# Performance work log

Measured on AMD Instinct MI355X. Metric: run time of the kernel, lower is better.

## Reference

```python
import jax, jax.numpy as jnp
import numpy as np

B, T, D = 2, 2048, 1024
H, HS = 16, 64
EPS = 1e-5

def _ln(x, g, b):
    m = jnp.mean(x, axis=-1, keepdims=True)
    v = jnp.mean((x - m) ** 2, axis=-1, keepdims=True)
    return (x - m) * jax.lax.rsqrt(v + EPS) * g + b

def setup_inputs() -> dict:
    key = jax.random.key(0)
    ks = jax.random.split(key, 8)
    s_in = 1.0 / np.sqrt(D)
    s_ff = 1.0 / np.sqrt(4 * D)
    return {
        "embds": jax.random.normal(ks[0], (B, T, D), jnp.float32),
        "Wq": jax.random.normal(ks[1], (H, D, HS), jnp.float32) * s_in,
        "Wk": jax.random.normal(ks[2], (H, D, HS), jnp.float32) * s_in,
        "Wv": jax.random.normal(ks[3], (H, D, HS), jnp.float32) * s_in,
        "ln1_g": jnp.ones((D,), jnp.float32),
        "ln1_b": jnp.zeros((D,), jnp.float32),
        "ln2_g": jnp.ones((D,), jnp.float32),
        "ln2_b": jnp.zeros((D,), jnp.float32),
        "W1": jax.random.normal(ks[4], (D, 4 * D), jnp.float32) * s_in,
        "b1": jnp.zeros((4 * D,), jnp.float32),
        "W2": jax.random.normal(ks[5], (4 * D, D), jnp.float32) * s_ff,
        "b2": jnp.zeros((D,), jnp.float32),
    }

def reference(embds, Wq, Wk, Wv, ln1_g, ln1_b, ln2_g, ln2_b, W1, b1, W2, b2):
    _, t, d = embds.shape
    x = _ln(embds, ln1_g, ln1_b)
    q = jnp.einsum("btd,hde->bhte", x, Wq)
    k = jnp.einsum("btd,hde->bhte", x, Wk)
    v = jnp.einsum("btd,hde->bhte", x, Wv)
    # NOTE: repo scales by num_embds**-0.5 (C of input), not head_size**-0.5
    scores = jnp.einsum("bhte,bhse->bhts", q, k) * (d ** -0.5)
    causal = jnp.tril(jnp.ones((t, t), bool))
    scores = jnp.where(causal, scores, -jnp.inf)
    w = jax.nn.softmax(scores, axis=-1)
    o = jnp.einsum("bhts,bhse->bhte", w, v)  # [B,H,T,HS]
    attn = o.transpose(0, 2, 1, 3).reshape(embds.shape[0], t, -1)  # concat heads
    embds = embds + attn
    y = _ln(embds, ln2_g, ln2_b)
    ff = jax.nn.relu(y @ W1 + b1) @ W2 + b2
    return embds + ff
```

## Files before the change

### kernel.cpp

```cpp
#include <hip/hip_runtime.h>

using s16x8 = __attribute__((ext_vector_type(8))) short;
using f32x4 = __attribute__((ext_vector_type(4))) float;
typedef unsigned int   u32;
typedef unsigned short u16;

__device__ __forceinline__ u16 f2bf(float f) {
  u32 u = __float_as_uint(f);
  u += 0x7fffu + ((u >> 16) & 1u);
  return (u16)(u >> 16);
}
__device__ __forceinline__ float bf2f(u16 s) {
  return __uint_as_float(((u32)s) << 16);
}

typedef __attribute__((address_space(1))) const unsigned int g_u32;
typedef __attribute__((address_space(3))) unsigned int l_u32;
__device__ __forceinline__ void gload16(const void* g, void* l) {
  __builtin_amdgcn_global_load_lds((g_u32*)g, (l_u32*)l, 16, 0, 0);
}

#define WAITB(N) asm volatile("s_waitcnt vmcnt(" #N ")\ns_barrier" ::: "memory")
#define BAR()    asm volatile("s_barrier" ::: "memory")

__device__ __forceinline__ size_t kfrag_addr(int bh, int t, int e) {
  const int pair = (((t >> 4) & 3) << 1) + (e >> 5);
  const int slot = ((e >> 3) & 3) * 16 + (t & 15);
  return ((((size_t)bh * 32 + (t >> 6)) * 8 + pair) * 64 + slot) * 8 + (e & 7);
}
__device__ __forceinline__ size_t vfrag_addr(int bh, int t, int e) {
  const int pair = (((e >> 4) & 3) << 1) + ((t >> 5) & 1);
  const int slot = ((t >> 3) & 3) * 16 + (e & 15);
  return ((((size_t)bh * 32 + (t >> 6)) * 8 + pair) * 64 + slot) * 8 + (t & 7);
}

__global__ __launch_bounds__(256) void transpose_pack(
    const float* __restrict__ src, u16* __restrict__ dst, int R, int C)
{
  __shared__ u16 tile[64][66];
  const int tid = threadIdx.x;
  const int c0 = blockIdx.x * 64, r0 = blockIdx.y * 64;
  const size_t zoff = (size_t)blockIdx.z * R * C;
  src += zoff; dst += zoff;
  const int rr = tid >> 6, cc = tid & 63;
  #pragma unroll
  for (int i = 0; i < 16; ++i)
    tile[i * 4 + rr][cc] = f2bf(src[(size_t)(r0 + i * 4 + rr) * C + c0 + cc]);
  __syncthreads();
  #pragma unroll
  for (int i = 0; i < 16; ++i)
    dst[(size_t)(c0 + i * 4 + rr) * R + r0 + cc] = tile[cc][i * 4 + rr];
}

__global__ __launch_bounds__(256) void transpose_qkv(
    const float* __restrict__ Wq, const float* __restrict__ Wk,
    const float* __restrict__ Wv, u16* __restrict__ dst)
{
  __shared__ u16 tile[64][66];
  const int tid = threadIdx.x;
  const int sel = blockIdx.z >> 4, head = blockIdx.z & 15;
  const int r0 = blockIdx.y * 64;
  const float* src = ((sel == 0) ? Wq : (sel == 1) ? Wk : Wv) + (size_t)head * 65536;
  u16* d = dst + ((size_t)sel << 20) + (size_t)head * 65536;
  const int rr = tid >> 6, cc = tid & 63;
  #pragma unroll
  for (int i = 0; i < 16; ++i)
    tile[i * 4 + rr][cc] = f2bf(src[(size_t)(r0 + i * 4 + rr) * 64 + cc]);
  __syncthreads();
  #pragma unroll
  for (int i = 0; i < 16; ++i)
    d[(size_t)(i * 4 + rr) * 1024 + r0 + cc] = tile[cc][i * 4 + rr];
}

__global__ __launch_bounds__(256) void ln_kernel(
    const float* __restrict__ x, const float* __restrict__ g,
    const float* __restrict__ be, u16* __restrict__ out)
{
  const int row = blockIdx.x, tid = threadIdx.x;
  const int lane = tid & 63, wave = tid >> 6;
  const float4 v = ((const float4*)(x + (size_t)row * 1024))[tid];
  float s  = v.x + v.y + v.z + v.w;
  float sq = v.x * v.x + v.y * v.y + v.z * v.z + v.w * v.w;
  #pragma unroll
  for (int m = 1; m < 64; m <<= 1) { s += __shfl_xor(s, m); sq += __shfl_xor(sq, m); }
  __shared__ float rs[4], rq[4];
  if (lane == 0) { rs[wave] = s; rq[wave] = sq; }
  __syncthreads();
  s  = rs[0] + rs[1] + rs[2] + rs[3];
  sq = rq[0] + rq[1] + rq[2] + rq[3];
  const float mean = s * (1.0f / 1024.0f);
  const float var  = sq * (1.0f / 1024.0f) - mean * mean;
  const float rstd = rsqrtf(var + 1e-5f);
  const int c = tid * 4;
  const float4 gv = ((const float4*)g)[tid];
  const float4 bv = ((const float4*)be)[tid];
  ushort4 o;
  o.x = f2bf((v.x - mean) * rstd * gv.x + bv.x);
  o.y = f2bf((v.y - mean) * rstd * gv.y + bv.y);
  o.z = f2bf((v.z - mean) * rstd * gv.z + bv.z);
  o.w = f2bf((v.w - mean) * rstd * gv.w + bv.w);
  *(ushort4*)&out[(size_t)row * 1024 + c] = o;
}

#define MFMA_Q(MQ, NH)                                                        \
  do {                                                                        \
    __builtin_amdgcn_s_setprio(1);                                            \
    _Pragma("unroll") for (int m_ = 0; m_ < 4; ++m_)                          \
      _Pragma("unroll") for (int n_ = 0; n_ < 2; ++n_)                        \
        _Pragma("unroll") for (int ks_ = 0; ks_ < 2; ++ks_)                   \
          acc[MQ * 4 + m_][NH * 2 + n_] =                                     \
            __builtin_amdgcn_mfma_f32_16x16x32_bf16(                          \
              aF[m_][ks_], (NH ? b1F : b0F)[n_][ks_],                         \
              acc[MQ * 4 + m_][NH * 2 + n_], 0, 0, 0);                        \
    __builtin_amdgcn_s_setprio(0);                                            \
  } while (0)

template<int MODE>
__global__ __launch_bounds__(512, 2) void gemm256(
    const u16* __restrict__ A, int lda, const u16* __restrict__ BT, int ldb,
    int K, u16* __restrict__ o1, const float* __restrict__ bias,
    u16* __restrict__ pout, u16* __restrict__ o0q, u16* __restrict__ o0k,
    u16* __restrict__ o0v)
{
  __shared__ alignas(16) u16 lds[2][2][256 * 64];
  const int tid = threadIdx.x, lane = tid & 63, w = tid >> 6;
  const int wm = w >> 2, wn = w & 3;
  const int fr = lane & 15, g = lane >> 4;
  const int gx = gridDim.x, nwg = gx * gridDim.y;
  int lid = blockIdx.y * gx + blockIdx.x;
  lid = (lid & 7) * (nwg >> 3) + (lid >> 3);
  const int col0 = (lid % gx) * 256, row0 = (lid / gx) * 256;
  const int koff = (MODE == 3) ? blockIdx.z * 1024 : 0;
  if constexpr (MODE == 3) pout += (size_t)blockIdx.z * (4096 * 1024);

  const int srow = w * 16 + (lane >> 3);
  const int scol8 = (lane & 7) ^ ((lane >> 3) & 7);
  const u16* Ab = A  + (size_t)(row0 + srow) * lda + koff + scol8 * 8;
  const u16* Bb = BT + (size_t)(col0 + srow) * ldb + koff + scol8 * 8;
  const int sdst = (w * 16) * 64 + lane * 8;

  const int x7 = fr & 7;
  const int rA = wm * 128 + fr;
  const int rB = wn * 64 + fr;

  f32x4 acc[8][4] = {};
  s16x8 aF[4][2], b0F[2][2], b1F[2][2];
  const int nkt = K >> 6;

  auto stA = [&](int buf, int half, int kt) {
    #pragma unroll
    for (int g2 = 0; g2 < 2; ++g2)
      gload16(Ab + (size_t)(half * 128 + g2 * 8) * lda + kt * 64,
              &lds[buf][0][(half * 128 + g2 * 8) * 64 + sdst]);
  };
  auto stB = [&](int buf, int half, int kt) {
    #pragma unroll
    for (int g2 = 0; g2 < 2; ++g2)
      gload16(Bb + (size_t)(half * 128 + g2 * 8) * ldb + kt * 64,
              &lds[buf][1][(half * 128 + g2 * 8) * 64 + sdst]);
  };
  auto rdA = [&](int buf, int mq) {
    #pragma unroll
    for (int m = 0; m < 4; ++m)
      #pragma unroll
      for (int ks = 0; ks < 2; ++ks)
        aF[m][ks] = *(const s16x8*)
          &lds[buf][0][(rA + mq * 64 + m * 16) * 64 + ((ks * 4 + g) ^ x7) * 8];
  };
  auto rdB0 = [&](int buf) {
    #pragma unroll
    for (int n = 0; n < 2; ++n)
      #pragma unroll
      for (int ks = 0; ks < 2; ++ks)
        b0F[n][ks] = *(const s16x8*)
          &lds[buf][1][(rB + n * 16) * 64 + ((ks * 4 + g) ^ x7) * 8];
  };
  auto rdB1 = [&](int buf) {
    #pragma unroll
    for (int n = 0; n < 2; ++n)
      #pragma unroll
      for (int ks = 0; ks < 2; ++ks)
        b1F[n][ks] = *(const s16x8*)
          &lds[buf][1][(rB + (n + 2) * 16) * 64 + ((ks * 4 + g) ^ x7) * 8];
  };

  stA(0, 0, 0); stA(0, 1, 0); stB(0, 0, 0); stB(0, 1, 0);
  stA(1, 0, 1); stA(1, 1, 1); stB(1, 0, 1); stB(1, 1, 1);
  WAITB(8);

  const int niter = nkt >> 1;
  for (int i = 0; i < niter; ++i) {
    #pragma unroll
    for (int half = 0; half < 2; ++half) {
      const int buf = half;
      const int skt = 2 * i + 2 + half;
      const bool st = (skt < nkt);
      rdA(buf, 0); rdB0(buf);
      BAR();
      MFMA_Q(0, 0);
      BAR();
      rdB1(buf);
      if (st) stB(buf, 0, skt);
      BAR();
      MFMA_Q(0, 1);
      BAR();
      rdA(buf, 1);
      if (st) stA(buf, 0, skt);
      BAR();
      MFMA_Q(1, 0);
      BAR();
      if (st) { stA(buf, 1, skt); stB(buf, 1, skt); }
      BAR();
      MFMA_Q(1, 1);
      WAITB(6);
    }
  }

  const float QSCALE = 0.03125f * 1.4426950408889634f;
  #pragma unroll
  for (int m8 = 0; m8 < 8; ++m8) {
    const int rbase = row0 + wm * 128 + m8 * 16 + g * 4;
    #pragma unroll
    for (int n4 = 0; n4 < 4; ++n4) {
      const int col = col0 + wn * 64 + n4 * 16 + fr;
      if constexpr (MODE == 0) {
        const int ww = col >> 10, h = (col >> 6) & 15, e = col & 63;
        const int b = rbase >> 11, t0 = rbase & 2047;
        const int bh = b * 16 + h;
        if (ww == 0) {
          #pragma unroll
          for (int j = 0; j < 4; ++j)
            o0q[((size_t)bh * 2048 + (t0 + j)) * 64 + e] =
              f2bf(acc[m8][n4][j] * QSCALE);
        } else if (ww == 1) {
          #pragma unroll
          for (int j = 0; j < 4; ++j)
            o0k[kfrag_addr(bh, t0 + j, e)] = f2bf(acc[m8][n4][j]);
        } else {
          ushort4 pk;
          pk.x = f2bf(acc[m8][n4][0]); pk.y = f2bf(acc[m8][n4][1]);
          pk.z = f2bf(acc[m8][n4][2]); pk.w = f2bf(acc[m8][n4][3]);
          *(ushort4*)&o0v[vfrag_addr(bh, t0, e)] = pk;
        }
      } else if constexpr (MODE == 1) {
        const float bb = bias[col];
        #pragma unroll
        for (int j = 0; j < 4; ++j)
          o1[(size_t)(rbase + j) * 4096 + col] =
            f2bf(fmaxf(acc[m8][n4][j] + bb, 0.0f));
      } else {
        #pragma unroll
        for (int j = 0; j < 4; ++j)
          pout[(size_t)(rbase + j) * 1024 + col] = f2bf(acc[m8][n4][j]);
      }
    }
  }
}

__global__ __launch_bounds__(256) void ff2_reduce(
    const u16* __restrict__ pbuf, const float* __restrict__ e2,
    const float* __restrict__ b2, float* __restrict__ out)
{
  const int i4 = blockIdx.x * 256 + threadIdx.x;
  const int row = i4 >> 8, c4 = i4 & 255;
  float4 a = ((const float4*)e2)[i4];
  const float4 bb = ((const float4*)b2)[c4];
  a.x += bb.x; a.y += bb.y; a.z += bb.z; a.w += bb.w;
  #pragma unroll
  for (int z = 0; z < 4; ++z) {
    const ushort4 p = *(const ushort4*)
      &pbuf[(size_t)z * (4096 * 1024) + (size_t)row * 1024 + c4 * 4];
    a.x += bf2f(p.x); a.y += bf2f(p.y); a.z += bf2f(p.z); a.w += bf2f(p.w);
  }
  ((float4*)out)[i4] = a;
}

__global__ __launch_bounds__(512, 6) void attn_mfma(
    const u16* __restrict__ q, const u16* __restrict__ kfragG,
    const u16* __restrict__ vfragG, const float* __restrict__ embds,
    float* __restrict__ e2)
{
  __shared__ alignas(16) u16 kbuf[2][4096];
  __shared__ alignas(16) u16 vbuf[2][4096];
  __shared__ alignas(16) u16 p_sm[8][16][72];
  const int tid = threadIdx.x, lane = tid & 63, wave = tid >> 6;
  const int bh = blockIdx.x & 31;
  const int qb = 15 - (blockIdx.x >> 5);
  const int q0 = qb * 128 + wave * 16;
  const int b = bh >> 4, h = bh & 15;
  const int fr = lane & 15, g = lane >> 4;

  const u16* qp = q + ((size_t)bh * 2048 + q0 + fr) * 64 + g * 8;
  const s16x8 qf0 = *(const s16x8*)(qp);
  const s16x8 qf1 = *(const s16x8*)(qp + 32);

  f32x4 o_acc[4] = {};
  float lacc[4] = {};

  const size_t fragbase = (size_t)bh * 131072;
  const int nch = qb * 2 + 2;

  auto stage_kv = [&](int sel, int c) {
    const size_t cb = fragbase + (size_t)c * 4096;
    gload16(kfragG + cb + wave * 512 + lane * 8, &kbuf[sel][wave * 512]);
    gload16(vfragG + cb + wave * 512 + lane * 8, &vbuf[sel][wave * 512]);
  };
  auto compute = [&](int sel, int s0) {
    f32x4 sacc[4] = {};
    #pragma unroll
    for (int n = 0; n < 4; ++n) {
      const s16x8 kf0 = *(const s16x8*)&kbuf[sel][(n * 2 + 0) * 512 + lane * 8];
      const s16x8 kf1 = *(const s16x8*)&kbuf[sel][(n * 2 + 1) * 512 + lane * 8];
      sacc[n] = __builtin_amdgcn_mfma_f32_16x16x32_bf16(qf0, kf0, sacc[n], 0, 0, 0);
      sacc[n] = __builtin_amdgcn_mfma_f32_16x16x32_bf16(qf1, kf1, sacc[n], 0, 0, 0);
    }
    if (s0 + 63 > q0) {
      #pragma unroll
      for (int n = 0; n < 4; ++n) {
        const int s = s0 + n * 16 + fr;
        #pragma unroll
        for (int j = 0; j < 4; ++j)
          if (s > q0 + g * 4 + j) sacc[n][j] = -1e30f;
      }
    }
    #pragma unroll
    for (int n = 0; n < 4; ++n)
      #pragma unroll
      for (int j = 0; j < 4; ++j) {
        const float pe = __builtin_amdgcn_exp2f(sacc[n][j]);
        lacc[j] += pe;
        p_sm[wave][g * 4 + j][n * 16 + fr] = f2bf(pe);
      }
    const s16x8 pf0 = *(const s16x8*)&p_sm[wave][fr][g * 8];
    const s16x8 pf1 = *(const s16x8*)&p_sm[wave][fr][32 + g * 8];
    #pragma unroll
    for (int n = 0; n < 4; ++n) {
      const s16x8 vf0 = *(const s16x8*)&vbuf[sel][(n * 2 + 0) * 512 + lane * 8];
      const s16x8 vf1 = *(const s16x8*)&vbuf[sel][(n * 2 + 1) * 512 + lane * 8];
      o_acc[n] = __builtin_amdgcn_mfma_f32_16x16x32_bf16(pf0, vf0, o_acc[n], 0, 0, 0);
      o_acc[n] = __builtin_amdgcn_mfma_f32_16x16x32_bf16(pf1, vf1, o_acc[n], 0, 0, 0);
    }
  };

  stage_kv(0, 0);
  for (int t = 0; t < nch; ++t) {
    WAITB(0);
    if (t + 1 < nch) stage_kv((t + 1) & 1, t + 1);
    compute(t & 1, t * 64);
  }

  #pragma unroll
  for (int j = 0; j < 4; ++j) {
    #pragma unroll
    for (int mm = 1; mm < 16; mm <<= 1) lacc[j] += __shfl_xor(lacc[j], mm);
  }
  #pragma unroll
  for (int n = 0; n < 4; ++n) {
    #pragma unroll
    for (int j = 0; j < 4; ++j) {
      const int t = q0 + g * 4 + j;
      const size_t oi = ((size_t)b * 2048 + t) * 1024 + (size_t)h * 64 + n * 16 + fr;
      e2[oi] = embds[oi] + o_acc[n][j] / lacc[j];
    }
  }
}

extern "C" void kernel_launch(void* const* d_in, const int* in_sizes, int n_in,
                              void* d_out, int out_size, void* d_ws, size_t ws_size,
                              hipStream_t stream) {
  const float* embds = (const float*)d_in[0];
  const float* Wq    = (const float*)d_in[1];
  const float* Wk    = (const float*)d_in[2];
  const float* Wv    = (const float*)d_in[3];
  const float* ln1g  = (const float*)d_in[4];
  const float* ln1b  = (const float*)d_in[5];
  const float* ln2g  = (const float*)d_in[6];
  const float* ln2b  = (const float*)d_in[7];
  const float* W1    = (const float*)d_in[8];
  const float* b1    = (const float*)d_in[9];
  const float* W2    = (const float*)d_in[10];
  const float* b2    = (const float*)d_in[11];
  float* out = (float*)d_out;

  char* ws = (char*)d_ws;
  u16*   xln   = (u16*)(ws);
  u16*   pbuf  = (u16*)(ws);
  u16*   wqkvT = (u16*)(ws + (8ull  << 20));
  u16*   qbuf  = (u16*)(ws + (14ull << 20));
  u16*   kfrag = (u16*)(ws + (22ull << 20));
  u16*   vfrag = (u16*)(ws + (30ull << 20));
  float* e2    = (float*)(ws + (38ull << 20));
  u16*   ybuf  = (u16*)(ws + (54ull << 20));
  u16*   w1T   = (u16*)(ws + (62ull << 20));
  u16*   w2T   = (u16*)(ws + (70ull << 20));
  u16*   hid   = (u16*)(ws + (78ull << 20));

  transpose_qkv<<<dim3(1, 16, 48), 256, 0, stream>>>(Wq, Wk, Wv, wqkvT);
  transpose_pack<<<dim3(64, 16, 1), 256, 0, stream>>>(W1, w1T, 1024, 4096);
  transpose_pack<<<dim3(16, 64, 1), 256, 0, stream>>>(W2, w2T, 4096, 1024);
  ln_kernel<<<4096, 256, 0, stream>>>(embds, ln1g, ln1b, xln);
  gemm256<0><<<dim3(12, 16), 512, 0, stream>>>(xln, 1024, wqkvT, 1024, 1024,
      nullptr, nullptr, nullptr, qbuf, kfrag, vfrag);
  attn_mfma<<<512, 512, 0, stream>>>(qbuf, kfrag, vfrag, embds, e2);
  ln_kernel<<<4096, 256, 0, stream>>>(e2, ln2g, ln2b, ybuf);
  gemm256<1><<<dim3(16, 16), 512, 0, stream>>>(ybuf, 1024, w1T, 1024, 1024,
      hid, b1, nullptr, nullptr, nullptr, nullptr);
  gemm256<3><<<dim3(4, 16, 4), 512, 0, stream>>>(hid, 4096, w2T, 4096, 1024,
      nullptr, nullptr, pbuf, nullptr, nullptr, nullptr);
  ff2_reduce<<<4096, 256, 0, stream>>>(pbuf, e2, b2, out);
}
```

Baseline: 191.5 us.

## Give each attention wave two 16-row query tiles to reuse K/V fragments

The attention kernel now runs 4 waves per block instead of 8, and each wave handles 32 query rows as two 16-row sub-tiles. K and V fragments are loaded once from LDS per chunk and reused across both sub-tiles, which halves LDS reads per MFMA. Each wave now issues two staging loads per tensor. The P scratch row padding also changes from 72 to 68. The cost is higher register pressure and fewer waves per block, which lowers latency hiding, and the launch-bounds occupancy hint changes to 2.

Measured after the change: 196.7 us. 1.03x slower.

```diff
diff --git a/kernel.cpp b/kernel.cpp
--- a/kernel.cpp
+++ b/kernel.cpp
@@ -275,70 +275,95 @@
   ((float4*)out)[i4] = a;
 }
 
-__global__ __launch_bounds__(512, 6) void attn_mfma(
+__global__ __launch_bounds__(256, 2) void attn_mfma(
     const u16* __restrict__ q, const u16* __restrict__ kfragG,
     const u16* __restrict__ vfragG, const float* __restrict__ embds,
     float* __restrict__ e2)
 {
   __shared__ alignas(16) u16 kbuf[2][4096];
   __shared__ alignas(16) u16 vbuf[2][4096];
-  __shared__ alignas(16) u16 p_sm[8][16][72];
+  __shared__ alignas(16) u16 p_sm[8][16][68];
   const int tid = threadIdx.x, lane = tid & 63, wave = tid >> 6;
   const int bh = blockIdx.x & 31;
   const int qb = 15 - (blockIdx.x >> 5);
-  const int q0 = qb * 128 + wave * 16;
+  const int q0 = qb * 128 + wave * 32;
   const int b = bh >> 4, h = bh & 15;
   const int fr = lane & 15, g = lane >> 4;
 
-  const u16* qp = q + ((size_t)bh * 2048 + q0 + fr) * 64 + g * 8;
-  const s16x8 qf0 = *(const s16x8*)(qp);
-  const s16x8 qf1 = *(const s16x8*)(qp + 32);
-
-  f32x4 o_acc[4] = {};
-  float lacc[4] = {};
+  s16x8 qf[2][2];
+  #pragma unroll
+  for (int u = 0; u < 2; ++u) {
+    const u16* qp = q + ((size_t)bh * 2048 + q0 + u * 16 + fr) * 64 + g * 8;
+    qf[u][0] = *(const s16x8*)(qp);
+    qf[u][1] = *(const s16x8*)(qp + 32);
+  }
+
+  f32x4 o_acc[2][4] = {};
+  float lacc[2][4] = {};
 
   const size_t fragbase = (size_t)bh * 131072;
   const int nch = qb * 2 + 2;
 
   auto stage_kv = [&](int sel, int c) {
     const size_t cb = fragbase + (size_t)c * 4096;
-    gload16(kfragG + cb + wave * 512 + lane * 8, &kbuf[sel][wave * 512]);
-    gload16(vfragG + cb + wave * 512 + lane * 8, &vbuf[sel][wave * 512]);
-  };
+    gload16(kfragG + cb + (wave * 2 + 0) * 512 + lane * 8, &kbuf[sel][(wave * 2 + 0) * 512]);
+    gload16(kfragG + cb + (wave * 2 + 1) * 512 + lane * 8, &kbuf[sel][(wave * 2 + 1) * 512]);
+    gload16(vfragG + cb + (wave * 2 + 0) * 512 + lane * 8, &vbuf[sel][(wave * 2 + 0) * 512]);
+    gload16(vfragG + cb + (wave * 2 + 1) * 512 + lane * 8, &vbuf[sel][(wave * 2 + 1) * 512]);
+  };
+
   auto compute = [&](int sel, int s0) {
-    f32x4 sacc[4] = {};
-    #pragma unroll
-    for (int n = 0; n < 4; ++n) {
-      const s16x8 kf0 = *(const s16x8*)&kbuf[sel][(n * 2 + 0) * 512 + lane * 8];
-      const s16x8 kf1 = *(const s16x8*)&kbuf[sel][(n * 2 + 1) * 512 + lane * 8];
-      sacc[n] = __builtin_amdgcn_mfma_f32_16x16x32_bf16(qf0, kf0, sacc[n], 0, 0, 0);
-      sacc[n] = __builtin_amdgcn_mfma_f32_16x16x32_bf16(qf1, kf1, sacc[n], 0, 0, 0);
-    }
-    if (s0 + 63 > q0) {
+    s16x8 kf[4][2];
+    #pragma unroll
+    for (int n = 0; n < 4; ++n)
+      #pragma unroll
+      for (int ks = 0; ks < 2; ++ks)
+        kf[n][ks] = *(const s16x8*)&kbuf[sel][(n * 2 + ks) * 512 + lane * 8];
+
+    #pragma unroll
+    for (int u = 0; u < 2; ++u) {
+      const int q0u = q0 + u * 16;
+      f32x4 sacc[4] = {};
       #pragma unroll
       for (int n = 0; n < 4; ++n) {
-        const int s = s0 + n * 16 + fr;
+        sacc[n] = __builtin_amdgcn_mfma_f32_16x16x32_bf16(qf[u][0], kf[n][0], sacc[n], 0, 0, 0);
+        sacc[n] = __builtin_amdgcn_mfma_f32_16x16x32_bf16(qf[u][1], kf[n][1], sacc[n], 0, 0, 0);
+      }
+      if (s0 + 63 > q0u) {
         #pragma unroll
-        for (int j = 0; j < 4; ++j)
-          if (s > q0 + g * 4 + j) sacc[n][j] = -1e30f;
+        for (int n = 0; n < 4; ++n) {
+          const int s = s0 + n * 16 + fr;
+          #pragma unroll
+          for (int j = 0; j < 4; ++j)
+            if (s > q0u + g * 4 + j) sacc[n][j] = -1e30f;
+        }
       }
-    }
+      #pragma unroll
+      for (int n = 0; n < 4; ++n)
+        #pragma unroll
+        for (int j = 0; j < 4; ++j) {
+          const float pe = __builtin_amdgcn_exp2f(sacc[n][j]);
+          lacc[u][j] += pe;
+          p_sm[wave * 2 + u][g * 4 + j][n * 16 + fr] = f2bf(pe);
+        }
+    }
+
+    s16x8 vf[4][2];
     #pragma unroll
     for (int n = 0; n < 4; ++n)
       #pragma unroll
-      for (int j = 0; j < 4; ++j) {
-        const float pe = __builtin_amdgcn_exp2f(sacc[n][j]);
-        lacc[j] += pe;
-        p_sm[wave][g * 4 + j][n * 16 + fr] = f2bf(pe);
+      for (int ks = 0; ks < 2; ++ks)
+        vf[n][ks] = *(const s16x8*)&vbuf[sel][(n * 2 + ks) * 512 + lane * 8];
+
+    #pragma unroll
+    for (int u = 0; u < 2; ++u) {
+      const s16x8 pf0 = *(const s16x8*)&p_sm[wave * 2 + u][fr][g * 8];
+      const s16x8 pf1 = *(const s16x8*)&p_sm[wave * 2 + u][fr][32 + g * 8];
+      #pragma unroll
+      for (int n = 0; n < 4; ++n) {
+        o_acc[u][n] = __builtin_amdgcn_mfma_f32_16x16x32_bf16(pf0, vf[n][0], o_acc[u][n], 0, 0, 0);
+        o_acc[u][n] = __builtin_amdgcn_mfma_f32_16x16x32_bf16(pf1, vf[n][1], o_acc[u][n], 0, 0, 0);
       }
-    const s16x8 pf0 = *(const s16x8*)&p_sm[wave][fr][g * 8];
-    const s16x8 pf1 = *(const s16x8*)&p_sm[wave][fr][32 + g * 8];
-    #pragma unroll
-    for (int n = 0; n < 4; ++n) {
-      const s16x8 vf0 = *(const s16x8*)&vbuf[sel][(n * 2 + 0) * 512 + lane * 8];
-      const s16x8 vf1 = *(const s16x8*)&vbuf[sel][(n * 2 + 1) * 512 + lane * 8];
-      o_acc[n] = __builtin_amdgcn_mfma_f32_16x16x32_bf16(pf0, vf0, o_acc[n], 0, 0, 0);
-      o_acc[n] = __builtin_amdgcn_mfma_f32_16x16x32_bf16(pf1, vf1, o_acc[n], 0, 0, 0);
     }
   };
 
@@ -350,19 +375,24 @@
   }
 
   #pragma unroll
-  for (int j = 0; j < 4; ++j) {
-    #pragma unroll
-    for (int mm = 1; mm < 16; mm <<= 1) lacc[j] += __shfl_xor(lacc[j], mm);
-  }
-  #pragma unroll
-  for (int n = 0; n < 4; ++n) {
+  for (int u = 0; u < 2; ++u)
     #pragma unroll
     for (int j = 0; j < 4; ++j) {
-      const int t = q0 + g * 4 + j;
-      const size_t oi = ((size_t)b * 2048 + t) * 1024 + (size_t)h * 64 + n * 16 + fr;
-      e2[oi] = embds[oi] + o_acc[n][j] / lacc[j];
-    }
-  }
+      #pragma unroll
+      for (int mm = 1; mm < 16; mm <<= 1) lacc[u][j] += __shfl_xor(lacc[u][j], mm);
+    }
+
+  #pragma unroll
+  for (int u = 0; u < 2; ++u)
+    #pragma unroll
+    for (int n = 0; n < 4; ++n) {
+      #pragma unroll
+      for (int j = 0; j < 4; ++j) {
+        const int t = q0 + u * 16 + g * 4 + j;
+        const size_t oi = ((size_t)b * 2048 + t) * 1024 + (size_t)h * 64 + n * 16 + fr;
+        e2[oi] = embds[oi] + o_acc[u][n][j] / lacc[u][j];
+      }
+    }
 }
 
 extern "C" void kernel_launch(void* const* d_in, const int* in_sizes, int n_in,
@@ -401,7 +431,7 @@
   ln_kernel<<<4096, 256, 0, stream>>>(embds, ln1g, ln1b, xln);
   gemm256<0><<<dim3(12, 16), 512, 0, stream>>>(xln, 1024, wqkvT, 1024, 1024,
       nullptr, nullptr, nullptr, qbuf, kfrag, vfrag);
-  attn_mfma<<<512, 512, 0, stream>>>(qbuf, kfrag, vfrag, embds, e2);
+  attn_mfma<<<512, 256, 0, stream>>>(qbuf, kfrag, vfrag, embds, e2);
   ln_kernel<<<4096, 256, 0, stream>>>(e2, ln2g, ln2b, ybuf);
   gemm256<1><<<dim3(16, 16), 512, 0, stream>>>(ybuf, 1024, w1T, 1024, 1024,
       hid, b1, nullptr, nullptr, nullptr, nullptr);
```

## Split causal attention over KV chunks with partial outputs and combine kernel

Applied to the files above, without the earlier changes.

Query blocks are now split along the key/value dimension into up to four segments of eight 64-key chunks. This gives 1280 workgroups of more even size instead of 512 heavily imbalanced ones, with the aim of improving load balance across compute units. Each segment writes unnormalised bf16 partial outputs and row sums. A new combine kernel sums them, normalises, and adds the residual. The cost is an extra launch, partial-buffer traffic and bf16 rounding of the partials. The design relies on the softmax having no running max (a fixed exponent base), so partial sums add directly.

Result: slower. 201.6 us (+5.3%).

```diff
diff --git a/kernel.cpp b/kernel.cpp
--- a/kernel.cpp
+++ b/kernel.cpp
@@ -277,17 +277,23 @@
 
 __global__ __launch_bounds__(512, 6) void attn_mfma(
     const u16* __restrict__ q, const u16* __restrict__ kfragG,
-    const u16* __restrict__ vfragG, const float* __restrict__ embds,
-    float* __restrict__ e2)
+    const u16* __restrict__ vfragG, u16* __restrict__ opart,
+    float* __restrict__ lpart)
 {
   __shared__ alignas(16) u16 kbuf[2][4096];
   __shared__ alignas(16) u16 vbuf[2][4096];
   __shared__ alignas(16) u16 p_sm[8][16][72];
   const int tid = threadIdx.x, lane = tid & 63, wave = tid >> 6;
   const int bh = blockIdx.x & 31;
-  const int qb = 15 - (blockIdx.x >> 5);
+  const int seg = 39 - (blockIdx.x >> 5);
+  int qb, z;
+  if (seg < 4)       { qb = seg;                 z = 0; }
+  else if (seg < 12) { qb = 4 + ((seg - 4) >> 1);  z = (seg - 4) & 1; }
+  else if (seg < 24) { qb = 8 + (seg - 12) / 3;    z = (seg - 12) % 3; }
+  else               { qb = 12 + ((seg - 24) >> 2); z = (seg - 24) & 3; }
   const int q0 = qb * 128 + wave * 16;
-  const int b = bh >> 4, h = bh & 15;
+  const int t0c = z * 8;
+  const int t1c = min(z * 8 + 8, 2 * qb + 2);
   const int fr = lane & 15, g = lane >> 4;
 
   const u16* qp = q + ((size_t)bh * 2048 + q0 + fr) * 64 + g * 8;
@@ -298,7 +304,6 @@
   float lacc[4] = {};
 
   const size_t fragbase = (size_t)bh * 131072;
-  const int nch = qb * 2 + 2;
 
   auto stage_kv = [&](int sel, int c) {
     const size_t cb = fragbase + (size_t)c * 4096;
@@ -342,10 +347,10 @@
     }
   };
 
-  stage_kv(0, 0);
-  for (int t = 0; t < nch; ++t) {
+  stage_kv(t0c & 1, t0c);
+  for (int t = t0c; t < t1c; ++t) {
     WAITB(0);
-    if (t + 1 < nch) stage_kv((t + 1) & 1, t + 1);
+    if (t + 1 < t1c) stage_kv((t + 1) & 1, t + 1);
     compute(t & 1, t * 64);
   }
 
@@ -354,14 +359,51 @@
     #pragma unroll
     for (int mm = 1; mm < 16; mm <<= 1) lacc[j] += __shfl_xor(lacc[j], mm);
   }
-  #pragma unroll
-  for (int n = 0; n < 4; ++n) {
-    #pragma unroll
-    for (int j = 0; j < 4; ++j) {
-      const int t = q0 + g * 4 + j;
-      const size_t oi = ((size_t)b * 2048 + t) * 1024 + (size_t)h * 64 + n * 16 + fr;
-      e2[oi] = embds[oi] + o_acc[n][j] / lacc[j];
-    }
+
+  const int slot = bh * 40 + seg;
+  u16* ob = opart + (size_t)slot * (128 * 64);
+  #pragma unroll
+  for (int n = 0; n < 4; ++n)
+    #pragma unroll
+    for (int j = 0; j < 4; ++j)
+      ob[(wave * 16 + g * 4 + j) * 64 + n * 16 + fr] = f2bf(o_acc[n][j]);
+  if (fr == 0) {
+    #pragma unroll
+    for (int j = 0; j < 4; ++j)
+      lpart[(size_t)slot * 128 + wave * 16 + g * 4 + j] = lacc[j];
+  }
+}
+
+__global__ __launch_bounds__(256) void attn_combine(
+    const u16* __restrict__ opart, const float* __restrict__ lpart,
+    const float* __restrict__ embds, float* __restrict__ e2)
+{
+  const int qb = blockIdx.x, h = blockIdx.y, b = blockIdx.z;
+  const int bh = b * 16 + h;
+  const int SEGOFF[16] = {0,1,2,3,4,6,8,10,12,15,18,21,24,28,32,36};
+  const int so = SEGOFF[qb];
+  const int ns = (qb < 4) ? 1 : (qb < 8) ? 2 : (qb < 12) ? 3 : 4;
+  const int slot0 = bh * 40 + so;
+  const int tid = threadIdx.x;
+  const int rl = tid >> 4, c4 = (tid & 15) * 4;
+  #pragma unroll
+  for (int pass = 0; pass < 8; ++pass) {
+    const int row = pass * 16 + rl;
+    float ox = 0, oy = 0, oz = 0, ow = 0, l = 0;
+    for (int zz = 0; zz < ns; ++zz) {
+      const ushort4 p = *(const ushort4*)
+        &opart[((size_t)(slot0 + zz) * 128 + row) * 64 + c4];
+      ox += bf2f(p.x); oy += bf2f(p.y); oz += bf2f(p.z); ow += bf2f(p.w);
+      l += lpart[(size_t)(slot0 + zz) * 128 + row];
+    }
+    const float inv = 1.0f / l;
+    const int t = qb * 128 + row;
+    const size_t oi = ((size_t)b * 2048 + t) * 1024 + (size_t)h * 64 + c4;
+    const float4 eb = *(const float4*)&embds[oi];
+    float4 r;
+    r.x = eb.x + ox * inv; r.y = eb.y + oy * inv;
+    r.z = eb.z + oz * inv; r.w = eb.w + ow * inv;
+    *(float4*)&e2[oi] = r;
   }
 }
 
@@ -384,16 +426,18 @@
 
   char* ws = (char*)d_ws;
   u16*   xln   = (u16*)(ws);
+  u16*   opart = (u16*)(ws);
+  float* lpart = (float*)(ws + (21ull << 20));
   u16*   pbuf  = (u16*)(ws);
   u16*   wqkvT = (u16*)(ws + (8ull  << 20));
-  u16*   qbuf  = (u16*)(ws + (14ull << 20));
-  u16*   kfrag = (u16*)(ws + (22ull << 20));
-  u16*   vfrag = (u16*)(ws + (30ull << 20));
-  float* e2    = (float*)(ws + (38ull << 20));
-  u16*   ybuf  = (u16*)(ws + (54ull << 20));
-  u16*   w1T   = (u16*)(ws + (62ull << 20));
-  u16*   w2T   = (u16*)(ws + (70ull << 20));
-  u16*   hid   = (u16*)(ws + (78ull << 20));
+  u16*   qbuf  = (u16*)(ws + (22ull << 20));
+  u16*   kfrag = (u16*)(ws + (30ull << 20));
+  u16*   vfrag = (u16*)(ws + (38ull << 20));
+  float* e2    = (float*)(ws + (46ull << 20));
+  u16*   ybuf  = (u16*)(ws + (62ull << 20));
+  u16*   w1T   = (u16*)(ws + (70ull << 20));
+  u16*   w2T   = (u16*)(ws + (78ull << 20));
+  u16*   hid   = (u16*)(ws + (86ull << 20));
 
   transpose_qkv<<<dim3(1, 16, 48), 256, 0, stream>>>(Wq, Wk, Wv, wqkvT);
   transpose_pack<<<dim3(64, 16, 1), 256, 0, stream>>>(W1, w1T, 1024, 4096);
@@ -401,7 +445,8 @@
   ln_kernel<<<4096, 256, 0, stream>>>(embds, ln1g, ln1b, xln);
   gemm256<0><<<dim3(12, 16), 512, 0, stream>>>(xln, 1024, wqkvT, 1024, 1024,
       nullptr, nullptr, nullptr, qbuf, kfrag, vfrag);
-  attn_mfma<<<512, 512, 0, stream>>>(qbuf, kfrag, vfrag, embds, e2);
+  attn_mfma<<<1280, 512, 0, stream>>>(qbuf, kfrag, vfrag, opart, lpart);
+  attn_combine<<<dim3(16, 16, 2), 256, 0, stream>>>(opart, lpart, embds, e2);
   ln_kernel<<<4096, 256, 0, stream>>>(e2, ln2g, ln2b, ybuf);
   gemm256<1><<<dim3(16, 16), 512, 0, stream>>>(ybuf, 1024, w1T, 1024, 1024,
       hid, b1, nullptr, nullptr, nullptr, nullptr);
```
